# Performance work log

Hardware: AMD Instinct MI355X
Metric: run time of the kernel (lower is better)

Reference implementation:

```python
import jax, jax.numpy as jnp
import numpy as np
from functools import partial

BN_EPS = 1e-5

def conv2d(x, w, pad):
    # x: [N,C,H,W], w: [O,I,kh,kw]
    return jax.lax.conv_general_dilated(
        x, w, window_strides=(1, 1), padding=((pad, pad), (pad, pad)),
        dimension_numbers=("NCHW", "OIHW", "NCHW"))

def bn_prelu(x, gamma, beta, mean, var, alpha):
    # eval-mode BatchNorm2d followed by single-parameter PReLU
    scale = gamma * jax.lax.rsqrt(var + BN_EPS)
    h = x * scale[None, :, None, None] + (beta - mean * scale)[None, :, None, None]
    return jnp.where(h >= 0, h, alpha * h)

def unfold3x3(x):
    # torch nn.Unfold(3, padding=1): output layout [N, C*9, H*W]
    N, C, H, W = x.shape
    xp = jnp.pad(x, ((0, 0), (0, 0), (1, 1), (1, 1)))
    patches = jnp.stack(
        [xp[:, :, i:i + H, j:j + W] for i in range(3) for j in range(3)],
        axis=2)  # [N, C, 9, H, W] -- row-major identical to [N, C*9, H*W]
    return patches

def setup_inputs() -> dict:
    key = jax.random.key(0)
    ks = jax.random.split(key, 16)
    N, C, H, W = 16, 256, 64, 64
    K2 = 9
    inp = {
        "x": jax.random.normal(ks[0], (N, C, H, W), jnp.float32),
        "y": jax.random.normal(ks[1], (N, C, H, W), jnp.float32),
        # gernerate_kernel_spatial[0]: Conv3x3 C->C + BN + PReLU
        "W1": jax.random.normal(ks[2], (C, C, 3, 3), jnp.float32) * 0.05,
        "g1": jax.random.normal(ks[3], (C,), jnp.float32) * 0.1 + 1.0,
        "b1": jax.random.normal(ks[4], (C,), jnp.float32) * 0.1,
        "m1": jax.random.normal(ks[5], (C,), jnp.float32) * 0.1,
        "v1": jax.random.uniform(ks[6], (C,), jnp.float32, 0.5, 1.5),
        "a1": jnp.float32(0.25),
        # gernerate_kernel_spatial[1]: Conv1x1 C->9 + BN + PReLU
        "W2": jax.random.normal(ks[7], (K2, C, 1, 1), jnp.float32) * 0.05,
        "g2": jax.random.normal(ks[8], (K2,), jnp.float32) * 0.1 + 1.0,
        "b2": jax.random.normal(ks[9], (K2,), jnp.float32) * 0.1,
        "m2": jax.random.normal(ks[10], (K2,), jnp.float32) * 0.1,
        "v2": jax.random.uniform(ks[11], (K2,), jnp.float32, 0.5, 1.5),
        "a2": jnp.float32(0.25),
    }
    return inp

def reference(x, y, W1, g1, b1, m1, v1, a1, W2, g2, b2, m2, v2, a2):
    N, C, H, W = x.shape
    # dynamic per-pixel 3x3 kernel from y: [N, 9, H, W]
    h = bn_prelu(conv2d(y, W1, pad=1), g1, b1, m1, v1, a1)
    kernel = bn_prelu(conv2d(h, W2, pad=0), g2, b2, m2, v2, a2)
    # kernel.reshape(N,9,H,W,1).permute(0,2,3,1,4) -> [N,H,W,9]
    kern = jnp.transpose(kernel, (0, 2, 3, 1))
    # unfold(x) is [N, C*9, H*W]; torch reshapes it ROW-MAJOR to [N,H,W,C,9]
    ux = unfold3x3(x).reshape(N, H, W, C, 9)
    # matmul [N,H,W,C,9] @ [N,H,W,9,1] -> squeeze -> permute to NCHW
    out = jnp.einsum("nhwck,nhwk->nchw", ux, kern)
    return out
```

## Files before the change

kernel.cpp:

```cpp
#include <hip/hip_runtime.h>
#include <hip/hip_bf16.h>

typedef __attribute__((ext_vector_type(8))) short bf16x8;
typedef __attribute__((ext_vector_type(4))) float f32x4;
typedef __attribute__((ext_vector_type(8))) unsigned short u16x8;
typedef __attribute__((ext_vector_type(4))) unsigned short u16x4;

#define BN_EPS 1e-5f

__device__ __forceinline__ unsigned short f2bf(float f) {
  unsigned int u = __float_as_uint(f);
  unsigned int r = u + 0x7FFFu + ((u >> 16) & 1u);
  return (unsigned short)(r >> 16);
}
__device__ __forceinline__ float bf2f(unsigned short u) {
  union { float f; unsigned int i; } v; v.i = ((unsigned int)u) << 16; return v.f;
}

__device__ __forceinline__ void async_ld16(const unsigned short* g, unsigned short* l) {
  __builtin_amdgcn_global_load_lds(
      (const __attribute__((address_space(1))) void*)g,
      (__attribute__((address_space(3))) void*)l, 16, 0, 0);
}

__global__ __launch_bounds__(256) void params_kernel(
    const float* __restrict__ g1, const float* __restrict__ b1,
    const float* __restrict__ m1, const float* __restrict__ v1,
    const float* __restrict__ W2, const float* __restrict__ g2,
    const float* __restrict__ b2, const float* __restrict__ m2,
    const float* __restrict__ v2,
    float* __restrict__ bias1, float* __restrict__ W2f, float* __restrict__ bias2)
{
  int t = threadIdx.x;
  {
    float s = g1[t] * rsqrtf(v1[t] + BN_EPS);
    bias1[t] = b1[t] - m1[t] * s;
  }
  for (int i = t; i < 2304; i += 256) {
    int j = i >> 8;
    float s2 = g2[j] * rsqrtf(v2[j] + BN_EPS);
    W2f[i] = W2[i] * s2;
  }
  if (t < 9) {
    float s2 = g2[t] * rsqrtf(v2[t] + BN_EPS);
    bias2[t] = b2[t] - m2[t] * s2;
  }
}

__global__ __launch_bounds__(256) void fold_w1_kernel(
    const float* __restrict__ W1, const float* __restrict__ g1,
    const float* __restrict__ v1, unsigned short* __restrict__ Bt)
{
  int o = blockIdx.x;
  int t = threadIdx.x;
  float s = g1[o] * rsqrtf(v1[o] + BN_EPS);
  const float* src = W1 + (size_t)o * 2304 + (size_t)t * 9;
  float wv[9];
  #pragma unroll
  for (int tap = 0; tap < 9; ++tap) wv[tap] = src[tap] * s;
  unsigned short* dst = Bt + (size_t)o * 2304 + t;
  #pragma unroll
  for (int tap = 0; tap < 9; ++tap) dst[tap * 256] = f2bf(wv[tap]);
}

__global__ __launch_bounds__(256) void border_zero_kernel(unsigned short* __restrict__ yTp)
{
  int n = blockIdx.x, t = threadIdx.x;
  size_t base = (size_t)n * 66 * 66 * 256;
  u16x8 z = (u16x8){0, 0, 0, 0, 0, 0, 0, 0};
  for (int i = t; i < 2112; i += 256) {
    *(u16x8*)(yTp + base + (size_t)i * 8) = z;
    *(u16x8*)(yTp + base + (size_t)65 * 66 * 256 + (size_t)i * 8) = z;
  }
  for (int i = t; i < 2048; i += 256) {
    int hh = 1 + (i >> 5);
    int off = (i & 31) * 8;
    *(u16x8*)(yTp + base + ((size_t)hh * 66 + 0) * 256 + off) = z;
    *(u16x8*)(yTp + base + ((size_t)hh * 66 + 65) * 256 + off) = z;
  }
}

__global__ __launch_bounds__(256) void transpose_pad_kernel(
    const float* __restrict__ y, unsigned short* __restrict__ yTp)
{
  __shared__ unsigned short T[64][68];
  int t = threadIdx.x;
  int nb = blockIdx.x; int n = nb >> 6, h = nb & 63;
  int w4 = (t & 15) * 4;
  int cl = t >> 4;
  for (int cb = 0; cb < 4; ++cb) {
    __syncthreads();
    #pragma unroll
    for (int r = 0; r < 4; ++r) {
      int c = cb * 64 + cl + r * 16;
      float4 v = *(const float4*)(y + ((((size_t)n * 256 + c) * 64 + h) << 6) + w4);
      u16x4 pv = { f2bf(v.x), f2bf(v.y), f2bf(v.z), f2bf(v.w) };
      *(u16x4*)&T[cl + r * 16][w4] = pv;
    }
    __syncthreads();
    size_t base = (((size_t)n * 66 + (h + 1)) * 66 + 1) * 256 + cb * 64;
    #pragma unroll
    for (int pass = 0; pass < 2; ++pass) {
      int w = pass * 32 + (t >> 3);
      int c8 = (t & 7) * 8;
      u16x8 o;
      #pragma unroll
      for (int i = 0; i < 8; ++i) o[i] = T[c8 + i][w];
      *(u16x8*)(yTp + base + (size_t)w * 256 + c8) = o;
    }
  }
}

__global__ __launch_bounds__(256, 2) void conv3x3_mfma_kernel(
    const unsigned short* __restrict__ yTp, const unsigned short* __restrict__ Bt,
    const float* __restrict__ bias1, const float* __restrict__ a1p,
    unsigned short* __restrict__ hT)
{
  __shared__ unsigned short Als[2][4][4][66][8];
  __shared__ unsigned short Bls[2][4][256][8];
  int tid = threadIdx.x;
  int w = tid >> 6, l = tid & 63;
  int lr = l & 15, quad = l >> 4;
  int wm = w >> 1, wn = w & 1;
  int bm = blockIdx.x;
  int n = bm >> 5, hb = (bm & 31) * 2;

  f32x4 acc[4][8];
  #pragma unroll
  for (int im = 0; im < 4; ++im)
    #pragma unroll
    for (int in_ = 0; in_ < 8; ++in_)
      acc[im][in_] = (f32x4){0.f, 0.f, 0.f, 0.f};

  const size_t nb66 = (size_t)n * 66;
  const unsigned short* gaRow = yTp + (((nb66 + hb + w) * 66) << 8);
  const unsigned short* gb0 = Bt + (size_t)(w * 64 + l) * 2304;

  auto stageA = [&](int chunk, int buf) {
    const unsigned short* ga = gaRow + ((size_t)l << 8) + chunk * 32;
    #pragma unroll
    for (int q = 0; q < 4; ++q)
      async_ld16(ga + q * 8, &Als[buf][q][w][0][0]);
    if (l < 2) {
      const unsigned short* ga2 = gaRow + ((size_t)(64 + l) << 8) + chunk * 32;
      #pragma unroll
      for (int q = 0; q < 4; ++q)
        async_ld16(ga2 + q * 8, &Als[buf][q][w][64][0]);
    }
  };
  auto stageB = [&](int tap, int chunk, int buf) {
    const unsigned short* gb = gb0 + tap * 256 + chunk * 32;
    #pragma unroll
    for (int q = 0; q < 4; ++q)
      async_ld16(gb + q * 8, &Bls[buf][q][w * 64][0]);
  };

  stageA(0, 0);
  stageB(0, 0, 0);
  __syncthreads();

  int ab = 0, bb = 0;
  #pragma unroll 1
  for (int c = 0; c < 8; ++c) {
    #pragma unroll 1
    for (int t = 0; t < 9; ++t) {
      if (t == 0 && c < 7) stageA(c + 1, ab ^ 1);
      if (t < 8) stageB(t + 1, c, bb ^ 1);
      else if (c < 7) stageB(0, c + 1, bb ^ 1);

      int ti = t / 3, tj = t - 3 * ti;
      bf16x8 af[4], bfr[8];
      #pragma unroll
      for (int im = 0; im < 4; ++im)
        af[im] = *(const bf16x8*)&Als[ab][quad][wm + ti][im * 16 + lr + tj][0];
      #pragma unroll
      for (int in_ = 0; in_ < 8; ++in_)
        bfr[in_] = *(const bf16x8*)&Bls[bb][quad][wn * 128 + in_ * 16 + lr][0];
      #pragma unroll
      for (int im = 0; im < 4; ++im)
        #pragma unroll
        for (int in_ = 0; in_ < 8; ++in_)
          acc[im][in_] = __builtin_amdgcn_mfma_f32_16x16x32_bf16(
              af[im], bfr[in_], acc[im][in_], 0, 0, 0);

      __syncthreads();
      bb ^= 1;
    }
    ab ^= 1;
  }

  float a1 = a1p[0];
  size_t pix0 = (size_t)bm * 128 + wm * 64;
  #pragma unroll
  for (int in_ = 0; in_ < 8; ++in_) {
    int c = wn * 128 + in_ * 16 + lr;
    float bs = bias1[c];
    #pragma unroll
    for (int im = 0; im < 4; ++im) {
      size_t m0 = pix0 + im * 16 + quad * 4;
      #pragma unroll
      for (int r = 0; r < 4; ++r) {
        float v = acc[im][in_][r] + bs;
        v = (v >= 0.f) ? v : a1 * v;
        hT[(m0 + r) * 256 + c] = f2bf(v);
      }
    }
  }
}

__global__ __launch_bounds__(256) void conv1x1_kernel(
    const unsigned short* __restrict__ hT, const float* __restrict__ W2f,
    const float* __restrict__ bias2, const float* __restrict__ a2p,
    float* __restrict__ kernP)
{
  __shared__ float w2s[2304];
  int t = threadIdx.x;
  for (int i = t; i < 2304; i += 256) w2s[i] = W2f[i];
  __syncthreads();
  int seg = t & 3;
  int pr = t >> 2;
  int p = blockIdx.x * 64 + pr;
  const unsigned short* hp = hT + (size_t)p * 256;
  float acc[9];
  #pragma unroll
  for (int j = 0; j < 9; ++j) acc[j] = 0.f;
  for (int c0 = seg * 8; c0 < 256; c0 += 32) {
    u16x8 hv = *(const u16x8*)(hp + c0);
    float hf[8];
    #pragma unroll
    for (int i = 0; i < 8; ++i) hf[i] = bf2f(hv[i]);
    #pragma unroll
    for (int j = 0; j < 9; ++j)
      #pragma unroll
      for (int i = 0; i < 8; ++i)
        acc[j] = fmaf(hf[i], w2s[j * 256 + c0 + i], acc[j]);
  }
  #pragma unroll
  for (int j = 0; j < 9; ++j) {
    acc[j] += __shfl_xor(acc[j], 1);
    acc[j] += __shfl_xor(acc[j], 2);
  }
  if (seg == 0) {
    float a2 = a2p[0];
    #pragma unroll
    for (int j = 0; j < 9; ++j) {
      float v = acc[j] + bias2[j];
      v = (v >= 0.f) ? v : a2 * v;
      kernP[j * 65536 + p] = v;
    }
  }
}

__global__ __launch_bounds__(256) void apply_dyn_kernel(
    const float* __restrict__ x, const float* __restrict__ kernP,
    float* __restrict__ out)
{
  __shared__ float xs[66 * 67];
  __shared__ float ks[9][16];
  int t = threadIdx.x;
  int b = blockIdx.x;
  int g = b & 3;
  int nh = b >> 2;
  int n = nh >> 6, hp = nh & 63;
  int c = 4 * hp + g;

  const float* xplane = x + (((size_t)n * 256 + c) << 12);
  for (int i = t; i < 1024; i += 256) {
    float4 v = *(const float4*)(xplane + i * 4);
    int row = i >> 4;
    int col = (i & 15) * 4;
    float* d = &xs[(row + 1) * 67 + col + 1];
    d[0] = v.x; d[1] = v.y; d[2] = v.z; d[3] = v.w;
  }
  if (t < 67) { xs[t] = 0.f; xs[65 * 67 + t] = 0.f; }
  if (t < 128) { int r = (t >> 1) + 1; int cc = (t & 1) * 65; xs[r * 67 + cc] = 0.f; }
  int pbase = n * 4096 + hp * 64 + g * 16;
  for (int i = t; i < 144; i += 256)
    ks[i / 16][i & 15] = kernP[(i / 16) * 65536 + pbase + (i & 15)];
  __syncthreads();

  int s = t & 15;
  int crow = t >> 4;
  float ksr[9];
  #pragma unroll
  for (int k2 = 0; k2 < 9; ++k2) ksr[k2] = ks[k2][s];

  int r0 = s * 2304 + crow * 144;
  int k0 = r0 >> 12;
  int rem0 = r0 & 4095;
  int wcol = rem0 & 63;
  int ti0 = (k0 >= 6) ? 2 : ((k0 >= 3) ? 1 : 0);
  int tj0 = k0 - 3 * ti0;
  int addr = (rem0 >> 6) * 67 + wcol + ti0 * 67 + tj0;
  int cnt = 4096 - rem0;
  int kN = k0 + 1;
  int tiN = (kN >= 6) ? 2 : ((kN >= 3) ? 1 : 0);
  int addrAtCross = tiN * 67 + (kN - 3 * tiN);

  size_t outIdx = (((size_t)n * 256 + crow * 16) << 12) + (hp << 6) + g * 16 + s;
  #pragma unroll 4
  for (int oi = 0; oi < 16; ++oi) {
    float acc = 0.f;
    #pragma unroll
    for (int k2 = 0; k2 < 9; ++k2) {
      acc = fmaf(xs[addr], ksr[k2], acc);
      ++wcol; ++addr;
      if (wcol == 64) { wcol = 0; addr += 3; }
      if (--cnt == 0) addr = addrAtCross;
    }
    out[outIdx + ((size_t)oi << 12)] = acc;
  }
}

extern "C" void kernel_launch(void* const* d_in, const int* in_sizes, int n_in,
                              void* d_out, int out_size, void* d_ws, size_t ws_size,
                              hipStream_t stream) {
  const float* x  = (const float*)d_in[0];
  const float* y  = (const float*)d_in[1];
  const float* W1 = (const float*)d_in[2];
  const float* g1 = (const float*)d_in[3];
  const float* b1 = (const float*)d_in[4];
  const float* m1 = (const float*)d_in[5];
  const float* v1 = (const float*)d_in[6];
  const float* a1 = (const float*)d_in[7];
  const float* W2 = (const float*)d_in[8];
  const float* g2 = (const float*)d_in[9];
  const float* b2 = (const float*)d_in[10];
  const float* m2 = (const float*)d_in[11];
  const float* v2 = (const float*)d_in[12];
  const float* a2 = (const float*)d_in[13];
  float* out = (float*)d_out;

  char* ws = (char*)d_ws;
  size_t off = 0;
  const size_t yTp_bytes = (size_t)16 * 66 * 66 * 256 * 2;
  unsigned short* yTp = (unsigned short*)(ws + off); off += yTp_bytes;
  unsigned short* Bt  = (unsigned short*)(ws + off); off += (size_t)589824 * 2;
  unsigned short* hT  = (unsigned short*)(ws + off); off += (size_t)16777216 * 2;
  float* kernP = (float*)(ws + off); off += (size_t)589824 * 4;
  float* bias1 = (float*)(ws + off); off += 1024;
  float* W2f   = (float*)(ws + off); off += 9216;
  float* bias2 = (float*)(ws + off); off += 64;

  params_kernel<<<1, 256, 0, stream>>>(g1, b1, m1, v1, W2, g2, b2, m2, v2,
                                       bias1, W2f, bias2);
  fold_w1_kernel<<<256, 256, 0, stream>>>(W1, g1, v1, Bt);
  border_zero_kernel<<<16, 256, 0, stream>>>(yTp);
  transpose_pad_kernel<<<1024, 256, 0, stream>>>(y, yTp);
  conv3x3_mfma_kernel<<<512, 256, 0, stream>>>(yTp, Bt, bias1, a1, hT);
  conv1x1_kernel<<<1024, 256, 0, stream>>>(hT, W2f, bias2, a2, kernP);
  apply_dyn_kernel<<<4096, 256, 0, stream>>>(x, kernP, out);
}
```

Baseline: 368.3 us.

## Re-layout padded input and weights into 8-channel blocks for coalesced async loads

```diff
diff --git a/kernel.cpp b/kernel.cpp
--- a/kernel.cpp
+++ b/kernel.cpp
@@ -55,28 +55,28 @@
   int t = threadIdx.x;
   float s = g1[o] * rsqrtf(v1[o] + BN_EPS);
   const float* src = W1 + (size_t)o * 2304 + (size_t)t * 9;
-  float wv[9];
-  #pragma unroll
-  for (int tap = 0; tap < 9; ++tap) wv[tap] = src[tap] * s;
-  unsigned short* dst = Bt + (size_t)o * 2304 + t;
-  #pragma unroll
-  for (int tap = 0; tap < 9; ++tap) dst[tap * 256] = f2bf(wv[tap]);
+  int chunk = t >> 5, q = (t >> 3) & 3, e = t & 7;
+  #pragma unroll
+  for (int tap = 0; tap < 9; ++tap) {
+    float wv = src[tap] * s;
+    Bt[((((size_t)tap * 8 + chunk) * 4 + q) * 256 + o) * 8 + e] = f2bf(wv);
+  }
 }
 
 __global__ __launch_bounds__(256) void border_zero_kernel(unsigned short* __restrict__ yTp)
 {
-  int n = blockIdx.x, t = threadIdx.x;
-  size_t base = (size_t)n * 66 * 66 * 256;
+  int p = blockIdx.x;
+  int t = threadIdx.x;
+  size_t base = (size_t)p * (66 * 66 * 8);
   u16x8 z = (u16x8){0, 0, 0, 0, 0, 0, 0, 0};
-  for (int i = t; i < 2112; i += 256) {
-    *(u16x8*)(yTp + base + (size_t)i * 8) = z;
-    *(u16x8*)(yTp + base + (size_t)65 * 66 * 256 + (size_t)i * 8) = z;
-  }
-  for (int i = t; i < 2048; i += 256) {
-    int hh = 1 + (i >> 5);
-    int off = (i & 31) * 8;
-    *(u16x8*)(yTp + base + ((size_t)hh * 66 + 0) * 256 + off) = z;
-    *(u16x8*)(yTp + base + ((size_t)hh * 66 + 65) * 256 + off) = z;
+  if (t < 66) {
+    *(u16x8*)(yTp + base + (size_t)t * 8) = z;
+    *(u16x8*)(yTp + base + ((size_t)65 * 66 + t) * 8) = z;
+  }
+  if (t >= 128 && t < 192) {
+    int hh = t - 127;
+    *(u16x8*)(yTp + base + ((size_t)hh * 66) * 8) = z;
+    *(u16x8*)(yTp + base + ((size_t)hh * 66 + 65) * 8) = z;
   }
 }
 
@@ -98,15 +98,15 @@
       *(u16x4*)&T[cl + r * 16][w4] = pv;
     }
     __syncthreads();
-    size_t base = (((size_t)n * 66 + (h + 1)) * 66 + 1) * 256 + cb * 64;
+    size_t base = ((((size_t)n * 32 + cb * 8) * 66 + (h + 1)) * 66 + 1) * 8;
     #pragma unroll
     for (int pass = 0; pass < 2; ++pass) {
       int w = pass * 32 + (t >> 3);
-      int c8 = (t & 7) * 8;
+      int c8 = t & 7;
       u16x8 o;
       #pragma unroll
-      for (int i = 0; i < 8; ++i) o[i] = T[c8 + i][w];
-      *(u16x8*)(yTp + base + (size_t)w * 256 + c8) = o;
+      for (int i = 0; i < 8; ++i) o[i] = T[c8 * 8 + i][w];
+      *(u16x8*)(yTp + base + ((size_t)c8 * (66 * 66) + w) * 8) = o;
     }
   }
 }
@@ -132,41 +132,46 @@
     for (int in_ = 0; in_ < 8; ++in_)
       acc[im][in_] = (f32x4){0.f, 0.f, 0.f, 0.f};
 
-  const size_t nb66 = (size_t)n * 66;
-  const unsigned short* gaRow = yTp + (((nb66 + hb + w) * 66) << 8);
-  const unsigned short* gb0 = Bt + (size_t)(w * 64 + l) * 2304;
+  const unsigned short* gaBase = yTp + (size_t)n * 32 * (66 * 66 * 8);
 
   auto stageA = [&](int chunk, int buf) {
-    const unsigned short* ga = gaRow + ((size_t)l << 8) + chunk * 32;
-    #pragma unroll
-    for (int q = 0; q < 4; ++q)
-      async_ld16(ga + q * 8, &Als[buf][q][w][0][0]);
+    int qg0 = chunk * 4;
+    #pragma unroll
+    for (int q = 0; q < 4; ++q) {
+      const unsigned short* ga = gaBase +
+          (((size_t)(qg0 + q) * 66 + (hb + w)) * 66 + l) * 8;
+      async_ld16(ga, &Als[buf][q][w][0][0]);
+    }
     if (l < 2) {
-      const unsigned short* ga2 = gaRow + ((size_t)(64 + l) << 8) + chunk * 32;
-      #pragma unroll
-      for (int q = 0; q < 4; ++q)
-        async_ld16(ga2 + q * 8, &Als[buf][q][w][64][0]);
+      #pragma unroll
+      for (int q = 0; q < 4; ++q) {
+        const unsigned short* ga = gaBase +
+            (((size_t)(qg0 + q) * 66 + (hb + w)) * 66 + 64 + l) * 8;
+        async_ld16(ga, &Als[buf][q][w][64][0]);
+      }
     }
   };
   auto stageB = [&](int tap, int chunk, int buf) {
-    const unsigned short* gb = gb0 + tap * 256 + chunk * 32;
-    #pragma unroll
-    for (int q = 0; q < 4; ++q)
-      async_ld16(gb + q * 8, &Bls[buf][q][w * 64][0]);
+    #pragma unroll
+    for (int q = 0; q < 4; ++q) {
+      const unsigned short* gb = Bt +
+          ((((size_t)tap * 8 + chunk) * 4 + q) * 256 + w * 64 + l) * 8;
+      async_ld16(gb, &Bls[buf][q][w * 64][0]);
+    }
   };
 
   stageA(0, 0);
   stageB(0, 0, 0);
-  __syncthreads();
 
   int ab = 0, bb = 0;
   #pragma unroll 1
   for (int c = 0; c < 8; ++c) {
     #pragma unroll 1
     for (int t = 0; t < 9; ++t) {
-      if (t == 0 && c < 7) stageA(c + 1, ab ^ 1);
+      __syncthreads();
       if (t < 8) stageB(t + 1, c, bb ^ 1);
       else if (c < 7) stageB(0, c + 1, bb ^ 1);
+      if (t == 0 && c < 7) stageA(c + 1, ab ^ 1);
 
       int ti = t / 3, tj = t - 3 * ti;
       bf16x8 af[4], bfr[8];
@@ -183,7 +188,6 @@
           acc[im][in_] = __builtin_amdgcn_mfma_f32_16x16x32_bf16(
               af[im], bfr[in_], acc[im][in_], 0, 0, 0);
 
-      __syncthreads();
       bb ^= 1;
     }
     ab ^= 1;
@@ -345,7 +349,7 @@
   params_kernel<<<1, 256, 0, stream>>>(g1, b1, m1, v1, W2, g2, b2, m2, v2,
                                        bias1, W2f, bias2);
   fold_w1_kernel<<<256, 256, 0, stream>>>(W1, g1, v1, Bt);
-  border_zero_kernel<<<16, 256, 0, stream>>>(yTp);
+  border_zero_kernel<<<512, 256, 0, stream>>>(yTp);
   transpose_pad_kernel<<<1024, 256, 0, stream>>>(y, yTp);
   conv3x3_mfma_kernel<<<512, 256, 0, stream>>>(yTp, Bt, bias1, a1, hT);
   conv1x1_kernel<<<1024, 256, 0, stream>>>(hT, W2f, bias2, a2, kernP);
```

New measurement: 324.5 us. -11.9%, faster.
